# Kernel optimization log

Measured on AMD Instinct MI355X. Metric: run time of the kernel, lower is better.

## Reference

```python
import jax, jax.numpy as jnp
import numpy as np

B, N_WIN, N, C = 32, 64, 64, 256          # batch, windows/img, tokens/window, dim
Wh, Ww = 8, 8                              # window_size
H_RES, W_RES = 64, 64                      # input_resolution
NUM_HEADS = 1


def _relative_coords():
    coords = np.stack(np.meshgrid(np.arange(Wh), np.arange(Ww), indexing='ij')).reshape(2, -1)
    rel = coords[:, :, None] - coords[:, None, :]   # [2, N, N]
    return rel[0].astype(np.int32), rel[1].astype(np.int32)  # radius, azimuth


def setup_inputs() -> dict:
    key = jax.random.key(0)
    ks = jax.random.split(key, 10)
    B_ = B * N_WIN
    radius_np, azimuth_np = _relative_coords()
    std = 0.02
    return {
        'x': jax.random.normal(ks[0], (B_, N, C), dtype=jnp.float32),
        'theta_max': jax.random.uniform(ks[1], (B,), dtype=jnp.float32) * np.float32(np.pi),
        'qkv_w': jax.random.normal(ks[2], (3 * C, C), dtype=jnp.float32) * std,
        'qkv_b': jnp.zeros((3 * C,), dtype=jnp.float32),
        'proj_w': jax.random.normal(ks[3], (C, C), dtype=jnp.float32) * std,
        'proj_b': jnp.zeros((C,), dtype=jnp.float32),
        'a_p': jax.random.normal(ks[4], (2 * Ww - 1, NUM_HEADS), dtype=jnp.float32) * std,
        'b_p': jax.random.normal(ks[5], (2 * Ww - 1, NUM_HEADS), dtype=jnp.float32) * std,
        'a_r': jax.random.normal(ks[6], (2 * Wh - 1, NUM_HEADS), dtype=jnp.float32) * std,
        'b_r': jax.random.normal(ks[7], (2 * Wh - 1, NUM_HEADS), dtype=jnp.float32) * std,
        'radius': jnp.asarray(radius_np),
        'azimuth': jnp.asarray(azimuth_np),
    }


def reference(x, theta_max, qkv_w, qkv_b, proj_w, proj_b, a_p, b_p, a_r, b_r, radius, azimuth):
    B_, n, c = x.shape
    head_dim = c // NUM_HEADS
    scale = head_dim ** -0.5

    qkv = (x @ qkv_w.T + qkv_b).reshape(B_, n, 3, NUM_HEADS, head_dim).transpose(2, 0, 3, 1, 4)
    q, k, v = qkv[0], qkv[1], qkv[2]            # each [B_, h, N, d]
    attn = jnp.einsum('bhnd,bhmd->bhnm', q * scale, k)

    # polar azimuth bias (torch negative-index wrap on the table)
    Tp = a_p.shape[0]
    aidx = jnp.where(azimuth < 0, azimuth + Tp, azimuth)
    azf = azimuth.astype(x.dtype) * (2.0 * np.pi / W_RES)        # [N, N]
    A_phi = a_p[aidx] * jnp.cos(azf)[..., None] + b_p[aidx] * jnp.sin(azf)[..., None]  # [N, N, h]
    bias_phi = jnp.transpose(A_phi, (2, 0, 1))[None]             # [1, h, N, N]

    # polar radius bias, modulated per-sample by theta_max
    Tr = a_r.shape[0]
    ridx = jnp.where(radius < 0, radius + Tr, radius)
    nW = B_ // theta_max.shape[0]
    tm = jnp.repeat(theta_max, nW).reshape(B_, 1, 1, 1)
    rnew = radius.astype(x.dtype)[None, :, :, None] * tm / H_RES  # [B_, N, N, 1]
    A_r = a_r[ridx][None] * jnp.cos(rnew) + b_r[ridx][None] * jnp.sin(rnew)  # [B_, N, N, h]
    A_theta = jnp.transpose(A_r, (0, 3, 1, 2))                   # [B_, h, N, N]

    attn = jax.nn.softmax(attn + bias_phi + A_theta, axis=-1)
    out = jnp.einsum('bhnm,bhmd->bhnd', attn, v).transpose(0, 2, 1, 3).reshape(B_, n, c)
    return out @ proj_w.T + proj_b
```

## Files before the change

kernel.cpp:

```cpp
#include <hip/hip_runtime.h>
#include <stdint.h>

#define NWINDOWS 2048

typedef short bf16x8 __attribute__((ext_vector_type(8)));
typedef float f32x4  __attribute__((ext_vector_type(4)));

#define OFF_WQKV  0u
#define OFF_WPROJ 393216u
#define OFF_BQKV  524288u
#define OFF_BIAS  527360u
#define OFF_QKV   1051648u
#define WS_NEED   202378240u

__device__ __forceinline__ unsigned short f2bf(float f) {
    union { float f; unsigned int u; } v; v.f = f;
    unsigned int u = v.u;
    u += 0x7FFFu + ((u >> 16) & 1u);
    return (unsigned short)(u >> 16);
}

__global__ __launch_bounds__(256)
void prep_kernel(const float* __restrict__ qkv_w, const float* __restrict__ qkv_b,
                 const float* __restrict__ proj_w, const float* __restrict__ theta_max,
                 const float* __restrict__ a_p, const float* __restrict__ b_p,
                 const float* __restrict__ a_r, const float* __restrict__ b_r,
                 const int* __restrict__ radius, const int* __restrict__ azimuth,
                 unsigned short* __restrict__ w_qkv, unsigned short* __restrict__ w_proj,
                 float* __restrict__ b_qkv, float* __restrict__ bias_tbl)
{
    int idx = blockIdx.x * 256 + threadIdx.x;
    const float scale = 0.0625f;
    if (idx < 196608) {
        int row = idx >> 8;
        float v = qkv_w[idx];
        if (row < 256) v *= scale;
        w_qkv[idx] = f2bf(v);
    } else if (idx < 196608 + 65536) {
        int j = idx - 196608;
        w_proj[j] = f2bf(proj_w[j]);
    } else if (idx < 196608 + 65536 + 768) {
        int j = idx - (196608 + 65536);
        float v = qkv_b[j];
        if (j < 256) v *= scale;
        b_qkv[j] = v;
    } else if (idx < 196608 + 65536 + 768 + 131072) {
        int j = idx - (196608 + 65536 + 768);
        int b  = j >> 12;
        int ij = j & 4095;
        int az = azimuth[ij];
        int rd = radius[ij];
        int aidx = az < 0 ? az + 15 : az;
        int ridx = rd < 0 ? rd + 15 : rd;
        float azf = (float)az * 0.09817477042468103f;
        float phi = a_p[aidx] * cosf(azf) + b_p[aidx] * sinf(azf);
        float rn  = (float)rd * theta_max[b] * 0.015625f;
        bias_tbl[j] = phi + a_r[ridx] * cosf(rn) + b_r[ridx] * sinf(rn);
    }
}

__global__ __launch_bounds__(256, 4)
void qkv_gemm(const float* __restrict__ x, const unsigned short* __restrict__ w_qkv,
              const float* __restrict__ b_qkv, unsigned short* __restrict__ qkv)
{
    __shared__ __align__(16) unsigned short Bs[2][16 * 256];
    __shared__ __align__(16) unsigned short Cp[4][32 * 72];

    const int tid  = threadIdx.x;
    const int w    = tid >> 6;
    const int lane = tid & 63;
    const int quad = lane >> 4;
    const int l16  = lane & 15;
    const int m3   = l16 & 7;
    const int mbase = blockIdx.x * 128 + w * 32;

    bf16x8 af[2][8];
    #pragma unroll
    for (int rt = 0; rt < 2; ++rt) {
        const float* xrow = x + (size_t)(mbase + rt * 16 + l16) * 256;
        #pragma unroll
        for (int kk = 0; kk < 8; ++kk) {
            const float4* p = (const float4*)(xrow + kk * 32 + quad * 8);
            float4 v0 = p[0], v1 = p[1];
            bf16x8 a;
            a[0] = (short)f2bf(v0.x); a[1] = (short)f2bf(v0.y);
            a[2] = (short)f2bf(v0.z); a[3] = (short)f2bf(v0.w);
            a[4] = (short)f2bf(v1.x); a[5] = (short)f2bf(v1.y);
            a[6] = (short)f2bf(v1.z); a[7] = (short)f2bf(v1.w);
            af[rt][kk] = a;
        }
    }

    const int srow = tid >> 5;
    const int sc   = (tid & 31) ^ (srow & 7);
    unsigned short* const db[2] = { &Bs[0][w * 512], &Bs[1][w * 512] };

    auto stage = [&](int nt, int buf) {
        const unsigned short* s0 = w_qkv + (nt * 16 + srow) * 256 + sc * 8;
        unsigned short* d = db[buf];
        __builtin_amdgcn_global_load_lds(
            (const __attribute__((address_space(1))) void*)s0,
            (__attribute__((address_space(3))) void*)d, 16, 0, 0);
        __builtin_amdgcn_global_load_lds(
            (const __attribute__((address_space(1))) void*)(s0 + 8 * 256),
            (__attribute__((address_space(3))) void*)(d + 2048), 16, 0, 0);
    };

    stage(0, 0);
    __syncthreads();

    const int rbase = l16 * 256;
    unsigned short* const cw = &Cp[w][0];
    const int frow = lane >> 3;
    const int fch  = lane & 7;

    for (int nt = 0; nt < 48; ++nt) {
        const int buf = nt & 1;
        if (nt + 1 < 48) stage(nt + 1, buf ^ 1);

        f32x4 acc0 = {0.f, 0.f, 0.f, 0.f};
        f32x4 acc1 = {0.f, 0.f, 0.f, 0.f};
        const unsigned short* bs = &Bs[buf][0] + rbase;
        #pragma unroll
        for (int kk = 0; kk < 8; ++kk) {
            int p = ((kk << 2) | quad) ^ m3;
            bf16x8 b = *(const bf16x8*)(bs + (p << 3));
            acc0 = __builtin_amdgcn_mfma_f32_16x16x32_bf16(af[0][kk], b, acc0, 0, 0, 0);
            acc1 = __builtin_amdgcn_mfma_f32_16x16x32_bf16(af[1][kk], b, acc1, 0, 0, 0);
        }

        const float bias = b_qkv[nt * 16 + l16];
        const int tcol = (nt & 3) * 16 + l16;
        #pragma unroll
        for (int r = 0; r < 4; ++r) {
            cw[(quad * 4 + r) * 72 + tcol]      = f2bf(acc0[r] + bias);
            cw[(16 + quad * 4 + r) * 72 + tcol] = f2bf(acc1[r] + bias);
        }

        if ((nt & 3) == 3) {
            const int colbase = (nt >> 2) * 64;
            #pragma unroll
            for (int i = 0; i < 4; ++i) {
                int row = i * 8 + frow;
                bf16x8 v = *(const bf16x8*)(cw + row * 72 + fch * 8);
                *(bf16x8*)(qkv + (size_t)(mbase + row) * 768 + colbase + fch * 8) = v;
            }
        }
        __syncthreads();
    }
}

__global__ __launch_bounds__(256, 2)
void attn_proj(const float* __restrict__ bias_tbl, const unsigned short* __restrict__ qkv,
               const unsigned short* __restrict__ w_proj, const float* __restrict__ proj_b,
               float* __restrict__ out)
{
    __shared__ unsigned short vT[256 * 64];
    __shared__ unsigned short Pl[64 * 72];
    __shared__ unsigned short Ol[64 * 264];

    const int win   = blockIdx.x;
    const int batch = win >> 6;
    const size_t rowbase = (size_t)win * 64;
    const int tid  = threadIdx.x;
    const int w    = tid >> 6;
    const int lane = tid & 63;
    const int quad = lane >> 4;
    const int l16  = lane & 15;

    {
        int tok  = tid >> 2;
        int part = tid & 3;
        const unsigned short* src = qkv + (rowbase + tok) * 768 + 512;
        #pragma unroll
        for (int jc = 0; jc < 8; ++jc) {
            int c = jc * 4 + part;
            bf16x8 v8 = *(const bf16x8*)(src + c * 8);
            #pragma unroll
            for (int e = 0; e < 8; ++e) {
                int d   = c * 8 + e;
                int swz = (((tok >> 3) ^ (d & 7)) << 3) | (tok & 7);
                vT[d * 64 + swz] = (unsigned short)v8[e];
            }
        }
    }

    bf16x8 qf[8];
    const unsigned short* qrow = qkv + (rowbase + w * 16 + l16) * 768;
    #pragma unroll
    for (int kk = 0; kk < 8; ++kk)
        qf[kk] = *(const bf16x8*)(qrow + kk * 32 + quad * 8);

    f32x4 S[4];
    #pragma unroll
    for (int t = 0; t < 4; ++t) {
        const unsigned short* krow = qkv + (rowbase + t * 16 + l16) * 768 + 256 + quad * 8;
        f32x4 c = {0.f, 0.f, 0.f, 0.f};
        #pragma unroll
        for (int kk = 0; kk < 8; ++kk) {
            bf16x8 b = *(const bf16x8*)(krow + kk * 32);
            c = __builtin_amdgcn_mfma_f32_16x16x32_bf16(qf[kk], b, c, 0, 0, 0);
        }
        S[t] = c;
    }

    const float* bt = bias_tbl + batch * 4096 + (w * 16 + quad * 4) * 64 + l16;
    #pragma unroll
    for (int t = 0; t < 4; ++t)
        #pragma unroll
        for (int r = 0; r < 4; ++r)
            S[t][r] += bt[r * 64 + t * 16];

    float inv[4];
    #pragma unroll
    for (int r = 0; r < 4; ++r) {
        float m = fmaxf(fmaxf(S[0][r], S[1][r]), fmaxf(S[2][r], S[3][r]));
        #pragma unroll
        for (int off = 1; off < 16; off <<= 1)
            m = fmaxf(m, __shfl_xor(m, off, 64));
        float s = 0.f;
        #pragma unroll
        for (int t = 0; t < 4; ++t) { S[t][r] = __expf(S[t][r] - m); s += S[t][r]; }
        #pragma unroll
        for (int off = 1; off < 16; off <<= 1)
            s += __shfl_xor(s, off, 64);
        inv[r] = 1.0f / s;
    }

    #pragma unroll
    for (int t = 0; t < 4; ++t)
        #pragma unroll
        for (int r = 0; r < 4; ++r)
            Pl[(w * 16 + quad * 4 + r) * 72 + t * 16 + l16] = f2bf(S[t][r] * inv[r]);

    __syncthreads();

    #pragma unroll
    for (int n = 0; n < 16; ++n) {
        f32x4 c = {0.f, 0.f, 0.f, 0.f};
        int dim = n * 16 + l16;
        #pragma unroll
        for (int kk = 0; kk < 2; ++kk) {
            bf16x8 a = *(const bf16x8*)(&Pl[(w * 16 + l16) * 72 + kk * 32 + quad * 8]);
            int chunk = (kk * 4 + quad) ^ (dim & 7);
            bf16x8 b = *(const bf16x8*)(&vT[dim * 64 + chunk * 8]);
            c = __builtin_amdgcn_mfma_f32_16x16x32_bf16(a, b, c, 0, 0, 0);
        }
        #pragma unroll
        for (int r = 0; r < 4; ++r)
            Ol[(w * 16 + quad * 4 + r) * 264 + dim] = f2bf(c[r]);
    }

    __syncthreads();

    bf16x8 af[4][8];
    #pragma unroll
    for (int rt = 0; rt < 4; ++rt)
        #pragma unroll
        for (int kk = 0; kk < 8; ++kk)
            af[rt][kk] = *(const bf16x8*)(&Ol[(rt * 16 + l16) * 264 + kk * 32 + quad * 8]);

    #pragma unroll
    for (int ntl = 0; ntl < 4; ++ntl) {
        int ncol = w * 64 + ntl * 16 + l16;
        const unsigned short* wp = w_proj + ncol * 256 + quad * 8;
        f32x4 acc[4] = {{0,0,0,0},{0,0,0,0},{0,0,0,0},{0,0,0,0}};
        #pragma unroll
        for (int kk = 0; kk < 8; ++kk) {
            bf16x8 b = *(const bf16x8*)(wp + kk * 32);
            #pragma unroll
            for (int rt = 0; rt < 4; ++rt)
                acc[rt] = __builtin_amdgcn_mfma_f32_16x16x32_bf16(af[rt][kk], b, acc[rt], 0, 0, 0);
        }
        float pb = proj_b[ncol];
        #pragma unroll
        for (int rt = 0; rt < 4; ++rt)
            #pragma unroll
            for (int r = 0; r < 4; ++r)
                out[(rowbase + rt * 16 + quad * 4 + r) * 256 + ncol] = acc[rt][r] + pb;
    }
}

extern "C" void kernel_launch(void* const* d_in, const int* in_sizes, int n_in,
                              void* d_out, int out_size, void* d_ws, size_t ws_size,
                              hipStream_t stream)
{
    const float* x       = (const float*)d_in[0];
    const float* theta   = (const float*)d_in[1];
    const float* qkv_w   = (const float*)d_in[2];
    const float* qkv_b   = (const float*)d_in[3];
    const float* proj_w  = (const float*)d_in[4];
    const float* proj_b  = (const float*)d_in[5];
    const float* a_p     = (const float*)d_in[6];
    const float* b_p     = (const float*)d_in[7];
    const float* a_r     = (const float*)d_in[8];
    const float* b_r     = (const float*)d_in[9];
    const int*   radius  = (const int*)d_in[10];
    const int*   azimuth = (const int*)d_in[11];

    if (ws_size < (size_t)WS_NEED) return;

    char* ws = (char*)d_ws;
    unsigned short* w_qkv    = (unsigned short*)(ws + OFF_WQKV);
    unsigned short* w_proj   = (unsigned short*)(ws + OFF_WPROJ);
    float*          b_qkv    = (float*)(ws + OFF_BQKV);
    float*          bias_tbl = (float*)(ws + OFF_BIAS);
    unsigned short* qkv      = (unsigned short*)(ws + OFF_QKV);

    prep_kernel<<<1540, 256, 0, stream>>>(qkv_w, qkv_b, proj_w, theta,
                                          a_p, b_p, a_r, b_r, radius, azimuth,
                                          w_qkv, w_proj, b_qkv, bias_tbl);
    qkv_gemm<<<1024, 256, 0, stream>>>(x, w_qkv, b_qkv, qkv);
    attn_proj<<<NWINDOWS, 256, 0, stream>>>(bias_tbl, qkv, w_proj, proj_b, (float*)d_out);
}
```

Measured before the change: 410.1 us.

## Pipeline QKV weight staging with 4-slot ring and vmcnt-based waits

After: 782.1 us. +90.7%, slower.

```diff
diff --git a/kernel.cpp b/kernel.cpp
--- a/kernel.cpp
+++ b/kernel.cpp
@@ -63,7 +63,7 @@
 void qkv_gemm(const float* __restrict__ x, const unsigned short* __restrict__ w_qkv,
               const float* __restrict__ b_qkv, unsigned short* __restrict__ qkv)
 {
-    __shared__ __align__(16) unsigned short Bs[2][16 * 256];
+    __shared__ __align__(16) unsigned short Bs[4][16 * 128];
     __shared__ __align__(16) unsigned short Cp[4][32 * 72];
 
     const int tid  = threadIdx.x;
@@ -91,54 +91,38 @@
         }
     }
 
-    const int srow = tid >> 5;
-    const int sc   = (tid & 31) ^ (srow & 7);
-    unsigned short* const db[2] = { &Bs[0][w * 512], &Bs[1][w * 512] };
-
-    auto stage = [&](int nt, int buf) {
-        const unsigned short* s0 = w_qkv + (nt * 16 + srow) * 256 + sc * 8;
-        unsigned short* d = db[buf];
+    const int srow = tid >> 4;
+    const int sc   = (tid & 15) ^ (srow & 7);
+    unsigned short* const lds0 = &Bs[0][0];
+
+    auto stage = [&](int h) {
+        const unsigned short* s0 =
+            w_qkv + ((h >> 1) * 16 + srow) * 256 + (h & 1) * 128 + sc * 8;
+        unsigned short* d = lds0 + (h & 3) * 2048 + tid * 8;
         __builtin_amdgcn_global_load_lds(
             (const __attribute__((address_space(1))) void*)s0,
             (__attribute__((address_space(3))) void*)d, 16, 0, 0);
-        __builtin_amdgcn_global_load_lds(
-            (const __attribute__((address_space(1))) void*)(s0 + 8 * 256),
-            (__attribute__((address_space(3))) void*)(d + 2048), 16, 0, 0);
     };
 
-    stage(0, 0);
-    __syncthreads();
-
-    const int rbase = l16 * 256;
+    stage(0); stage(1); stage(2);
+
     unsigned short* const cw = &Cp[w][0];
     const int frow = lane >> 3;
     const int fch  = lane & 7;
 
-    for (int nt = 0; nt < 48; ++nt) {
-        const int buf = nt & 1;
-        if (nt + 1 < 48) stage(nt + 1, buf ^ 1);
-
-        f32x4 acc0 = {0.f, 0.f, 0.f, 0.f};
-        f32x4 acc1 = {0.f, 0.f, 0.f, 0.f};
-        const unsigned short* bs = &Bs[buf][0] + rbase;
-        #pragma unroll
-        for (int kk = 0; kk < 8; ++kk) {
-            int p = ((kk << 2) | quad) ^ m3;
-            bf16x8 b = *(const bf16x8*)(bs + (p << 3));
-            acc0 = __builtin_amdgcn_mfma_f32_16x16x32_bf16(af[0][kk], b, acc0, 0, 0, 0);
-            acc1 = __builtin_amdgcn_mfma_f32_16x16x32_bf16(af[1][kk], b, acc1, 0, 0, 0);
-        }
-
-        const float bias = b_qkv[nt * 16 + l16];
-        const int tcol = (nt & 3) * 16 + l16;
-        #pragma unroll
-        for (int r = 0; r < 4; ++r) {
-            cw[(quad * 4 + r) * 72 + tcol]      = f2bf(acc0[r] + bias);
-            cw[(16 + quad * 4 + r) * 72 + tcol] = f2bf(acc1[r] + bias);
-        }
-
-        if ((nt & 3) == 3) {
-            const int colbase = (nt >> 2) * 64;
+    f32x4 acc0 = {0.f, 0.f, 0.f, 0.f};
+    f32x4 acc1 = {0.f, 0.f, 0.f, 0.f};
+
+    for (int h = 0; h < 96; ++h) {
+        if (h < 94)      asm volatile("s_waitcnt vmcnt(2)" ::: "memory");
+        else if (h == 94) asm volatile("s_waitcnt vmcnt(1)" ::: "memory");
+        else              asm volatile("s_waitcnt vmcnt(0)" ::: "memory");
+        __builtin_amdgcn_sched_barrier(0);
+        __builtin_amdgcn_s_barrier();
+        __builtin_amdgcn_sched_barrier(0);
+
+        if (h > 0 && (h & 7) == 0) {
+            const int colbase = (h >> 3) * 64 - 64;
             #pragma unroll
             for (int i = 0; i < 4; ++i) {
                 int row = i * 8 + frow;
@@ -146,7 +130,45 @@
                 *(bf16x8*)(qkv + (size_t)(mbase + row) * 768 + colbase + fch * 8) = v;
             }
         }
-        __syncthreads();
+        if (h + 3 < 96) stage(h + 3);
+        __builtin_amdgcn_sched_barrier(0);
+
+        if ((h & 1) == 0) {
+            acc0 = (f32x4){0.f, 0.f, 0.f, 0.f};
+            acc1 = (f32x4){0.f, 0.f, 0.f, 0.f};
+        }
+        const unsigned short* bsr = lds0 + (h & 3) * 2048 + l16 * 128;
+        const int ko = (h & 1) * 4;
+        __builtin_amdgcn_s_setprio(1);
+        #pragma unroll
+        for (int kk = 0; kk < 4; ++kk) {
+            int p = ((kk << 2) | quad) ^ m3;
+            bf16x8 b = *(const bf16x8*)(bsr + (p << 3));
+            acc0 = __builtin_amdgcn_mfma_f32_16x16x32_bf16(af[0][ko + kk], b, acc0, 0, 0, 0);
+            acc1 = __builtin_amdgcn_mfma_f32_16x16x32_bf16(af[1][ko + kk], b, acc1, 0, 0, 0);
+        }
+        __builtin_amdgcn_s_setprio(0);
+
+        if (h & 1) {
+            const int nt = h >> 1;
+            const float bias = b_qkv[nt * 16 + l16];
+            const int tcol = (nt & 3) * 16 + l16;
+            #pragma unroll
+            for (int r = 0; r < 4; ++r) {
+                cw[(quad * 4 + r) * 72 + tcol]      = f2bf(acc0[r] + bias);
+                cw[(16 + quad * 4 + r) * 72 + tcol] = f2bf(acc1[r] + bias);
+            }
+        }
+    }
+
+    {
+        const int colbase = 704;
+        #pragma unroll
+        for (int i = 0; i < 4; ++i) {
+            int row = i * 8 + frow;
+            bf16x8 v = *(const bf16x8*)(cw + row * 72 + fch * 8);
+            *(bf16x8*)(qkv + (size_t)(mbase + row) * 768 + colbase + fch * 8) = v;
+        }
     }
 }
 
```
